# Performance work log

Measured on AMD Instinct MI355X. Metric: run time of the kernel, lower is better.

The kernel has to match this reference:

```python
import jax, jax.numpy as jnp
import numpy as np

N, E, EP = 200000, 1600000, 1000000
D, H1, CH, XDIM, L = 64, 256, 128, 20, 3


def gelu(x):
    return jax.nn.gelu(x, approximate=False)  # torch default = exact erf GELU


def dyt(x, w, b, a):
    # DynamicTanh (channels_last): w * tanh(alpha * x) + b
    return w * jnp.tanh(a * x) + b


def graph_norm(x, w, b, ms, eps=1e-5):
    # PyG GraphNorm with a single graph (batch = all zeros)
    mean = jnp.mean(x, axis=0, keepdims=True)
    xc = x - ms * mean
    var = jnp.mean(xc * xc, axis=0, keepdims=True)
    return w * xc / jnp.sqrt(var + eps) + b


def setup_inputs() -> dict:
    key = jax.random.key(0)
    ks = iter(jax.random.split(key, 64))
    nrm = lambda shape, s: jax.random.normal(next(ks), shape, jnp.float32) * s
    d = {}
    d['x_res'] = nrm((N, D), 1.0)
    s = 1.0 / np.sqrt(D)
    d['Wl'] = nrm((L, D, D), s); d['bl'] = jnp.zeros((L, D)); d['Wr'] = nrm((L, D, D), s)
    d['gn_w'] = jnp.ones((L, D)); d['gn_b'] = jnp.zeros((L, D)); d['gn_ms'] = jnp.ones((L, D))
    d['dyt1_w'] = jnp.ones((L * D,)); d['dyt1_b'] = jnp.zeros((L * D,)); d['dyt1_a'] = jnp.full((1,), 0.5, jnp.float32)
    d['lin1_w'] = nrm((L * D, H1), 1.0 / np.sqrt(L * D)); d['lin1_b'] = jnp.zeros((H1,))
    d['lin2_w'] = nrm((H1, H1), 1.0 / np.sqrt(H1)); d['lin2_b'] = jnp.zeros((H1,))
    d['lin3_w'] = nrm((H1, D), 1.0 / np.sqrt(H1)); d['lin3_b'] = jnp.zeros((D,))
    d['dyt2_w'] = jnp.ones((D,)); d['dyt2_b'] = jnp.zeros((D,)); d['dyt2_a'] = jnp.full((1,), 0.5, jnp.float32)
    d['adyt1_w'] = jnp.ones((2 * D,)); d['adyt1_b'] = jnp.zeros((2 * D,)); d['adyt1_a'] = jnp.full((1,), 0.5, jnp.float32)
    d['aa1_w'] = nrm((2 * D, H1), 1.0 / np.sqrt(2 * D)); d['aa1_b'] = jnp.zeros((H1,))
    d['aa2_w'] = nrm((H1, H1), 1.0 / np.sqrt(H1)); d['aa2_b'] = jnp.zeros((H1,))
    d['aa3_w'] = nrm((H1, H1), 1.0 / np.sqrt(H1)); d['aa3_b'] = jnp.zeros((H1,))
    d['adyt2_w'] = jnp.ones((H1,)); d['adyt2_b'] = jnp.zeros((H1,)); d['adyt2_a'] = jnp.full((1,), 0.5, jnp.float32)
    d['aa4_w'] = nrm((H1, XDIM), 1.0 / np.sqrt(H1)); d['aa4_b'] = jnp.zeros((XDIM,))
    d['c1_w'] = nrm((2 * D, CH), 1.0 / np.sqrt(2 * D)); d['c1_b'] = jnp.zeros((CH,))
    d['c2_w'] = nrm((CH, CH), 1.0 / np.sqrt(CH)); d['c2_b'] = jnp.zeros((CH,))
    d['c3_w'] = nrm((CH, 1), 1.0 / np.sqrt(CH)); d['c3_b'] = jnp.zeros((1,))
    d['edge_index'] = jax.random.randint(next(ks), (2, E), 0, N, dtype=jnp.int64 if jax.config.jax_enable_x64 else jnp.int32).astype(jnp.int32)
    d['contact_pred_index'] = jax.random.randint(next(ks), (2, EP), 0, N).astype(jnp.int32)
    return d


def reference(x_res, Wl, bl, Wr, gn_w, gn_b, gn_ms, dyt1_w, dyt1_b, dyt1_a,
              lin1_w, lin1_b, lin2_w, lin2_b, lin3_w, lin3_b, dyt2_w, dyt2_b, dyt2_a,
              adyt1_w, adyt1_b, adyt1_a, aa1_w, aa1_b, aa2_w, aa2_b, aa3_w, aa3_b,
              adyt2_w, adyt2_b, adyt2_a, aa4_w, aa4_b,
              c1_w, c1_b, c2_w, c2_b, c3_w, c3_b, edge_index, contact_pred_index):
    n = x_res.shape[0]
    src, dst = edge_index[0], edge_index[1]
    inz = x_res  # dropout is identity in eval / p~0
    x = x_res
    # in-degree for SAGE mean aggregation (clamped to 1 like PyG)
    deg = jnp.maximum(jax.ops.segment_sum(jnp.ones_like(src, dtype=x.dtype), dst, num_segments=n), 1.0)[:, None]
    xs = []
    for i in range(Wl.shape[0]):
        prev = x
        agg = jax.ops.segment_sum(x[src], dst, num_segments=n) / deg  # [N, D] mean of neighbor messages
        h = agg @ Wl[i] + bl[i] + x @ Wr[i]                            # SAGEConv: lin_l(aggr) + lin_r(x_dst)
        h = gelu(h)
        h = graph_norm(h, gn_w[i], gn_b[i], gn_ms[i])
        if i > 0:
            h = h + prev  # residual from layer 1 onward
        x = h
        xs.append(x)
    z = jnp.concatenate(xs, axis=1)  # JumpingKnowledge 'cat' -> [N, 3*D]
    z = dyt(z, dyt1_w, dyt1_b, dyt1_a)
    z = gelu(z @ lin1_w + lin1_b)
    z = gelu(z @ lin2_w + lin2_b)
    z = gelu(z @ lin3_w + lin3_b)
    z = dyt(z, dyt2_w, dyt2_b, dyt2_a)
    z = z + inz                                   # residual=True
    z = z / (jnp.linalg.norm(z, axis=1, keepdims=True) + 1e-10)  # normalize=True
    dec_in = jnp.concatenate([inz, z], axis=1)    # [N, 2*D]
    a = dyt(dec_in, adyt1_w, adyt1_b, adyt1_a)
    a = gelu(a @ aa1_w + aa1_b)
    a = gelu(a @ aa2_w + aa2_b)
    a = gelu(a @ aa3_w + aa3_b)
    a = dyt(a, adyt2_w, adyt2_b, adyt2_a)
    aa = jax.nn.log_softmax(a @ aa4_w + aa4_b, axis=1)  # [N, 20]
    ci, cj = contact_pred_index[0], contact_pred_index[1]
    ce = jnp.concatenate([z[ci], z[cj]], axis=1)  # [EP, 2*D] gather
    ce = gelu(ce @ c1_w + c1_b)
    ce = gelu(ce @ c2_w + c2_b)
    edge_probs = jax.nn.sigmoid((ce @ c3_w + c3_b)[:, 0])  # [EP]
    return aa, edge_probs
```

## Files before the change

### kernel.cpp

```cpp
#include <hip/hip_runtime.h>
#include <cstdint>
#include <cstddef>

constexpr int Nn  = 200000;
constexpr int Ee  = 1600000;
constexpr int EPp = 1000000;

typedef __attribute__((ext_vector_type(8))) short bf8_t;
typedef __attribute__((ext_vector_type(4))) float f4_t;

__device__ inline unsigned short f2bf(float f) {
  union { float f; unsigned u; } v; v.f = f;
  unsigned r = v.u + 0x7FFFu + ((v.u >> 16) & 1u);
  return (unsigned short)(r >> 16);
}
__device__ inline float bf2f(unsigned short u) {
  union { unsigned u; float f; } v; v.u = ((unsigned)u) << 16;
  return v.f;
}
__device__ inline float gelu_f(float v) {
  float u = v * fmaf(0.0356774081f, v * v, 0.7978845608f);
  float r = __builtin_amdgcn_rcpf(__expf(u + u) + 1.0f);
  return fmaf(-v, r, v);
}
__device__ inline float dyt_f(float x, float s2, float w, float b) {
  float r = __builtin_amdgcn_rcpf(__expf(s2 * x) + 1.0f);
  return fmaf(w, fmaf(-2.0f, r, 1.0f), b);
}


__global__ __launch_bounds__(256) void k_degi(const int* __restrict__ dst,
                                              int* __restrict__ cnt, int E) {
  int i = blockIdx.x * 256 + threadIdx.x;
  if (i < E) atomicAdd(&cnt[dst[i]], 1);
}

__global__ __launch_bounds__(256) void k_scan1(const int* __restrict__ in,
                                               int* __restrict__ out,
                                               int* __restrict__ bsum,
                                               float* __restrict__ rdeg, int n) {
  __shared__ int sd[256];
  int t = threadIdx.x;
  int base = blockIdx.x * 1024 + t * 4;
  int v[4]; int ts = 0;
  #pragma unroll
  for (int j = 0; j < 4; ++j) { v[j] = (base + j < n) ? in[base + j] : 0; ts += v[j]; }
  sd[t] = ts; __syncthreads();
  for (int off = 1; off < 256; off <<= 1) {
    int x = (t >= off) ? sd[t - off] : 0;
    __syncthreads();
    sd[t] += x;
    __syncthreads();
  }
  int excl = sd[t] - ts;
  #pragma unroll
  for (int j = 0; j < 4; ++j) {
    if (base + j < n) {
      out[base + j] = excl;
      rdeg[base + j] = 1.0f / (float)(v[j] > 1 ? v[j] : 1);
    }
    excl += v[j];
  }
  if (t == 255) bsum[blockIdx.x] = sd[255];
}

__global__ void k_scan2(int* bsum, int nb) {
  __shared__ int sd[256];
  int t = threadIdx.x;
  int v = (t < nb) ? bsum[t] : 0;
  sd[t] = v; __syncthreads();
  for (int off = 1; off < 256; off <<= 1) {
    int x = (t >= off) ? sd[t - off] : 0;
    __syncthreads();
    sd[t] += x;
    __syncthreads();
  }
  if (t < nb) bsum[t] = sd[t] - v;
}

__global__ __launch_bounds__(256) void k_scan3(const int* __restrict__ part,
                                               const int* __restrict__ bsum,
                                               int* __restrict__ rowptr,
                                               int* __restrict__ cursor,
                                               int n, int total) {
  int i = blockIdx.x * 256 + threadIdx.x;
  if (i == 0) rowptr[n] = total;
  if (i < n) { int v = part[i] + bsum[i >> 10]; rowptr[i] = v; cursor[i] = v; }
}

__global__ __launch_bounds__(256) void k_fill(const int* __restrict__ src,
                                              const int* __restrict__ dst,
                                              int* __restrict__ cursor,
                                              int* __restrict__ colidx, int E) {
  int e = blockIdx.x * 256 + threadIdx.x;
  if (e >= E) return;
  int pos = atomicAdd(&cursor[dst[e]], 1);
  colidx[pos] = src[e];
}

__global__ __launch_bounds__(256) void k_gather(const unsigned short* __restrict__ x, int ldx,
                                                const int* __restrict__ rowptr,
                                                const int* __restrict__ colidx,
                                                const float* __restrict__ rdeg,
                                                unsigned short* __restrict__ agg, int n) {
  int wave = threadIdx.x >> 6, lane = threadIdx.x & 63;
  int node = blockIdx.x * 4 + wave;
  if (node >= n) return;
  int grp = lane >> 3, c = (lane & 7) * 8;
  int r0 = rowptr[node], r1 = rowptr[node + 1];
  float s[8] = {0.f, 0.f, 0.f, 0.f, 0.f, 0.f, 0.f, 0.f};
  for (int j = r0 + grp; j < r1; j += 8) {
    bf8_t v = *(const bf8_t*)(x + (size_t)colidx[j] * ldx + c);
    #pragma unroll
    for (int jj = 0; jj < 8; ++jj) s[jj] += bf2f((unsigned short)v[jj]);
  }
  #pragma unroll
  for (int jj = 0; jj < 8; ++jj) {
    s[jj] += __shfl_xor(s[jj], 8, 64);
    s[jj] += __shfl_xor(s[jj], 16, 64);
    s[jj] += __shfl_xor(s[jj], 32, 64);
  }
  if (grp == 0) {
    float r = rdeg[node];
    bf8_t o;
    #pragma unroll
    for (int jj = 0; jj < 8; ++jj) o[jj] = (short)f2bf(s[jj] * r);
    *(bf8_t*)(agg + (size_t)node * 64 + c) = o;
  }
}


__global__ __launch_bounds__(256) void k_cvt(const float* __restrict__ in,
                                             unsigned short* __restrict__ out, int n) {
  int i = blockIdx.x * 256 + threadIdx.x;
  if (i < n) out[i] = f2bf(in[i]);
}

__device__ inline void wt3_elem(const float* __restrict__ W,
                                unsigned short* __restrict__ Wt,
                                int Np, int Nr, int i) {
  int kin = i & 31;
  int j = i >> 5;
  int n = j % Np, kb = j / Np;
  int k = kb * 32 + kin;
  float v = (n < Nr) ? W[(size_t)k * Nr + n] : 0.f;
  Wt[i] = f2bf(v);
}
__device__ inline void wt2_elem(const float* __restrict__ W,
                                unsigned short* __restrict__ Wt,
                                int K, int N, int i) {
  int n = i / K, k = i - n * K;
  float v = (n < N) ? W[(size_t)k * N + n] : 0.f;
  Wt[i] = f2bf(v);
}

__global__ __launch_bounds__(256) void k_wtall(
    const float* __restrict__ Wl, const float* __restrict__ Wr,
    const float* __restrict__ lin1_w, const float* __restrict__ lin2_w,
    const float* __restrict__ lin3_w,
    const float* __restrict__ aa1_w, const float* __restrict__ aa2_w,
    const float* __restrict__ aa3_w, const float* __restrict__ aa4_w,
    const float* __restrict__ c1_w, const float* __restrict__ c2_w,
    unsigned short* __restrict__ wt_sage,
    unsigned short* __restrict__ wt_lin1, unsigned short* __restrict__ wt_lin2,
    unsigned short* __restrict__ wt_lin3,
    unsigned short* __restrict__ wt_aa1, unsigned short* __restrict__ wt_aa2,
    unsigned short* __restrict__ wt_aa3, unsigned short* __restrict__ wt_aa4,
    unsigned short* __restrict__ wt_c1, unsigned short* __restrict__ wt_c2) {
  int i = blockIdx.x * 256 + threadIdx.x;
  if (i < 24576) {
    int l = i >> 13, r = i & 8191, n = r >> 7, k = r & 127;
    float v = (k < 64) ? Wl[l * 4096 + k * 64 + n] : Wr[l * 4096 + (k - 64) * 64 + n];
    wt_sage[i] = f2bf(v);
    return;
  }
  i -= 24576;
  if (i < 49152) { wt3_elem(lin1_w, wt_lin1, 256, 256, i); return; }  i -= 49152;
  if (i < 65536) { wt3_elem(lin2_w, wt_lin2, 256, 256, i); return; }  i -= 65536;
  if (i < 16384) { wt3_elem(lin3_w, wt_lin3, 64, 64, i);   return; }  i -= 16384;
  if (i < 32768) { wt3_elem(aa1_w, wt_aa1, 256, 256, i);   return; }  i -= 32768;
  if (i < 65536) { wt3_elem(aa2_w, wt_aa2, 256, 256, i);   return; }  i -= 65536;
  if (i < 65536) { wt3_elem(aa3_w, wt_aa3, 256, 256, i);   return; }  i -= 65536;
  if (i < 8192)  { wt3_elem(aa4_w, wt_aa4, 32, 20, i);     return; }  i -= 8192;
  if (i < 16384) { wt2_elem(c1_w, wt_c1, 128, 128, i);     return; }  i -= 16384;
  if (i < 16384) { wt2_elem(c2_w, wt_c2, 128, 128, i);     return; }
}

__global__ void k_statfin(float* stats, const float* __restrict__ ms_, int n) {
  int d = threadIdx.x;
  if (d < 64) {
    float invn = 1.0f / (float)n;
    float m  = stats[d] * invn;
    float e2 = stats[64 + d] * invn;
    float ms = ms_[d];
    float var = e2 - (2.0f * ms - ms * ms) * m * m;
    stats[128 + d] = ms * m;
    stats[192 + d] = rsqrtf(var + 1e-5f);
  }
}

__global__ __launch_bounds__(256) void k_norm(const float* __restrict__ h,
                                              const float* __restrict__ stats,
                                              const float* __restrict__ w,
                                              const float* __restrict__ b,
                                              unsigned short* __restrict__ zcol,
                                              const unsigned short* __restrict__ prev, int n) {
  int i = blockIdx.x * 256 + threadIdx.x;
  if (i >= n * 64) return;
  int r = i >> 6, d = i & 63;
  float v = (h[i] - stats[128 + d]) * stats[192 + d] * w[d] + b[d];
  if (prev) v += bf2f(prev[(size_t)r * 192 + d]);
  zcol[(size_t)r * 192 + d] = f2bf(v);
}

template <int NT>
__global__ __launch_bounds__(256) void mgemm(
    const void* __restrict__ A1, int lda1,
    const void* __restrict__ A2, int lda2, int K1, int a_bf16,
    const unsigned short* __restrict__ Wt,
    const float* __restrict__ bias,
    void* __restrict__ Cout, int ldc, int c_bf16, int act,
    float* __restrict__ stats_out,
    int M, int K, int N) {
  int lane = threadIdx.x & 63, wave = threadIdx.x >> 6;
  int quad = lane >> 4, col = lane & 15;
  int row0 = blockIdx.x * 128 + wave * 32;
  int n_base = blockIdx.y * NT * 16;

  __shared__ float ls[128];
  if (stats_out) {
    if (threadIdx.x < 128) ls[threadIdx.x] = 0.f;
    __syncthreads();
  }

  f4_t acc[2][NT];
  #pragma unroll
  for (int mt = 0; mt < 2; ++mt)
    #pragma unroll
    for (int nt = 0; nt < NT; ++nt) acc[mt][nt] = (f4_t)0.f;

  int gm[2];
  gm[0] = row0 + col;      if (gm[0] >= M) gm[0] = M - 1;
  gm[1] = row0 + 16 + col; if (gm[1] >= M) gm[1] = M - 1;

  for (int kc0 = 0; kc0 < K; kc0 += 32) {
    int kc = kc0 + quad * 8;
    bf8_t a[2];
    #pragma unroll
    for (int mt = 0; mt < 2; ++mt) {
      const void* src; size_t off;
      if (kc < K1) { src = A1; off = (size_t)gm[mt] * lda1 + kc; }
      else         { src = A2; off = (size_t)gm[mt] * lda2 + kc - K1; }
      if (a_bf16) {
        a[mt] = *(const bf8_t*)((const unsigned short*)src + off);
      } else {
        const float* p = (const float*)src + off;
        float4 f0 = *(const float4*)p;
        float4 f1 = *(const float4*)(p + 4);
        float ff[8] = {f0.x, f0.y, f0.z, f0.w, f1.x, f1.y, f1.z, f1.w};
        #pragma unroll
        for (int j = 0; j < 8; ++j) a[mt][j] = (short)f2bf(ff[j]);
      }
    }
    #pragma unroll
    for (int nt = 0; nt < NT; ++nt) {
      bf8_t b = *(const bf8_t*)(Wt + (size_t)(n_base + nt * 16 + col) * K + kc);
      acc[0][nt] = __builtin_amdgcn_mfma_f32_16x16x32_bf16(a[0], b, acc[0][nt], 0, 0, 0);
      acc[1][nt] = __builtin_amdgcn_mfma_f32_16x16x32_bf16(a[1], b, acc[1][nt], 0, 0, 0);
    }
  }

  #pragma unroll
  for (int nt = 0; nt < NT; ++nt) {
    int n = n_base + nt * 16 + col;
    float bs = (bias && n < N) ? bias[n] : 0.f;
    float sa = 0.f, s2a = 0.f;
    #pragma unroll
    for (int mt = 0; mt < 2; ++mt)
      #pragma unroll
      for (int r = 0; r < 4; ++r) {
        int row = row0 + mt * 16 + quad * 4 + r;
        if (row >= M || n >= N) continue;
        float v = acc[mt][nt][r] + bs;
        if (act) v = gelu_f(v);
        sa += v; s2a += v * v;
        if (c_bf16) ((unsigned short*)Cout)[(size_t)row * ldc + n] = f2bf(v);
        else        ((float*)Cout)[(size_t)row * ldc + n] = v;
      }
    if (stats_out && n < N) {
      atomicAdd(&ls[n & 63], sa);
      atomicAdd(&ls[64 + (n & 63)], s2a);
    }
  }
  if (stats_out) {
    __syncthreads();
    if (threadIdx.x < 128) atomicAdd(&stats_out[threadIdx.x], ls[threadIdx.x]);
  }
}

template <int K, bool DYT>
__device__ inline void node_gemm(unsigned short (*H)[264],
                                 const unsigned short* __restrict__ W,
                                 const float* __restrict__ bias,
                                 int wave, int quad, int col,
                                 const float* __restrict__ a2w,
                                 const float* __restrict__ a2b,
                                 const float* __restrict__ aal) {
  constexpr int KS = K >> 5;
  f4_t acc[4][4];
  #pragma unroll
  for (int mt = 0; mt < 4; ++mt)
    #pragma unroll
    for (int nt = 0; nt < 4; ++nt) acc[mt][nt] = (f4_t)0.f;

  const unsigned short* wp = W + (size_t)(wave * 64 + col) * 32 + quad * 8;
  bf8_t bc[4];
  #pragma unroll
  for (int nt = 0; nt < 4; ++nt)
    bc[nt] = *(const bf8_t*)(wp + (size_t)(nt * 16) * 32);

  #pragma unroll 2
  for (int s = 0; s < KS; ++s) {
    bf8_t am[4];
    #pragma unroll
    for (int mt = 0; mt < 4; ++mt)
      am[mt] = *(const bf8_t*)&H[mt * 16 + col][s * 32 + quad * 8];
    bf8_t bn[4];
    if (s + 1 < KS) {
      #pragma unroll
      for (int nt = 0; nt < 4; ++nt)
        bn[nt] = *(const bf8_t*)(wp + (size_t)((s + 1) * 256 + nt * 16) * 32);
    }
    #pragma unroll
    for (int nt = 0; nt < 4; ++nt)
      #pragma unroll
      for (int mt = 0; mt < 4; ++mt)
        acc[mt][nt] = __builtin_amdgcn_mfma_f32_16x16x32_bf16(am[mt], bc[nt], acc[mt][nt], 0, 0, 0);
    if (s + 1 < KS) {
      #pragma unroll
      for (int nt = 0; nt < 4; ++nt) bc[nt] = bn[nt];
    }
  }
  __syncthreads();
  float sa = DYT ? (2.0f * aal[0]) : 0.f;
  #pragma unroll
  for (int nt = 0; nt < 4; ++nt) {
    int n = wave * 64 + nt * 16 + col;
    float bs = bias[n];
    float w_ = DYT ? a2w[n] : 0.f;
    float b_ = DYT ? a2b[n] : 0.f;
    #pragma unroll
    for (int mt = 0; mt < 4; ++mt)
      #pragma unroll
      for (int r4 = 0; r4 < 4; ++r4) {
        float v = gelu_f(acc[mt][nt][r4] + bs);
        if (DYT) v = dyt_f(v, sa, w_, b_);
        H[mt * 16 + quad * 4 + r4][n] = f2bf(v);
      }
  }
  __syncthreads();
}

__global__ __launch_bounds__(256, 3) void k_node(
    const unsigned short* __restrict__ z_bf,
    const float* __restrict__ x_res,
    const float* __restrict__ d1w, const float* __restrict__ d1b, const float* __restrict__ d1a,
    const unsigned short* __restrict__ wt1, const float* __restrict__ b1,
    const unsigned short* __restrict__ wt2, const float* __restrict__ b2,
    const unsigned short* __restrict__ wt3, const float* __restrict__ b3,
    const float* __restrict__ d2w, const float* __restrict__ d2b, const float* __restrict__ d2a,
    const float* __restrict__ a1w, const float* __restrict__ a1b, const float* __restrict__ a1a,
    const unsigned short* __restrict__ wa1, const float* __restrict__ ba1,
    const unsigned short* __restrict__ wa2, const float* __restrict__ ba2,
    const unsigned short* __restrict__ wa3, const float* __restrict__ ba3,
    const float* __restrict__ a2w, const float* __restrict__ a2b, const float* __restrict__ a2a,
    const unsigned short* __restrict__ wa4, const float* __restrict__ ba4,
    unsigned short* __restrict__ zn_bf,
    float* __restrict__ out, int M) {
  __shared__ unsigned short H[64][264];
  __shared__ float fscr[64 * 4 + 64];
  int t = threadIdx.x;
  int lane = t & 63, wave = t >> 6;
  int quad = lane >> 4, col = lane & 15;
  int brow = blockIdx.x * 64;

  {
    int row = t >> 2, part = t & 3;
    int gr = brow + row; if (gr >= M) gr = M - 1;
    const unsigned short* zp = z_bf + (size_t)gr * 192 + part * 48;
    float s1 = 2.0f * d1a[0];
    #pragma unroll
    for (int j = 0; j < 6; ++j) {
      bf8_t v = *(const bf8_t*)(zp + j * 8);
      int k0 = part * 48 + j * 8;
      #pragma unroll
      for (int jj = 0; jj < 8; ++jj) {
        float f = bf2f((unsigned short)v[jj]);
        v[jj] = (short)f2bf(dyt_f(f, s1, d1w[k0 + jj], d1b[k0 + jj]));
      }
      *(bf8_t*)&H[row][k0] = v;
    }
  }
  __syncthreads();

  node_gemm<192, false>(H, wt1, b1, wave, quad, col, nullptr, nullptr, nullptr);
  node_gemm<256, false>(H, wt2, b2, wave, quad, col, nullptr, nullptr, nullptr);

  {
    f4_t a3[4];
    #pragma unroll
    for (int mt = 0; mt < 4; ++mt) a3[mt] = (f4_t)0.f;
    const unsigned short* wp3 = wt3 + (size_t)(wave * 16 + col) * 32 + quad * 8;
    bf8_t bc = *(const bf8_t*)(wp3);
    #pragma unroll 2
    for (int s = 0; s < 8; ++s) {
      bf8_t am[4];
      #pragma unroll
      for (int mt = 0; mt < 4; ++mt)
        am[mt] = *(const bf8_t*)&H[mt * 16 + col][s * 32 + quad * 8];
      bf8_t bn;
      if (s + 1 < 8) bn = *(const bf8_t*)(wp3 + (size_t)((s + 1) * 64) * 32);
      #pragma unroll
      for (int mt = 0; mt < 4; ++mt)
        a3[mt] = __builtin_amdgcn_mfma_f32_16x16x32_bf16(am[mt], bc, a3[mt], 0, 0, 0);
      if (s + 1 < 8) bc = bn;
    }
    __syncthreads();
    float* fb = (float*)H;
    float s2d = 2.0f * d2a[0];
    int n = wave * 16 + col;
    float bsn = b3[n], wd = d2w[n], bd = d2b[n];
    #pragma unroll
    for (int mt = 0; mt < 4; ++mt)
      #pragma unroll
      for (int r4 = 0; r4 < 4; ++r4) {
        int row = mt * 16 + quad * 4 + r4;
        int gr = brow + row; if (gr >= M) gr = M - 1;
        float g = gelu_f(a3[mt][r4] + bsn);
        float x = x_res[(size_t)gr * 64 + n];
        fb[row * 66 + n] = dyt_f(g, s2d, wd, bd) + x;
      }
    __syncthreads();
    int row = t >> 2, q = t & 3;
    float vreg[16];
    float s2 = 0.f;
    #pragma unroll
    for (int c16 = 0; c16 < 16; ++c16) {
      vreg[c16] = fb[row * 66 + q * 16 + c16];
      s2 += vreg[c16] * vreg[c16];
    }
    fscr[row * 4 + q] = s2;
    __syncthreads();
    if (t < 64)
      fscr[256 + t] = 1.0f / (sqrtf(fscr[t * 4] + fscr[t * 4 + 1] + fscr[t * 4 + 2] + fscr[t * 4 + 3]) + 1e-10f);
    __syncthreads();
    float sa1 = 2.0f * a1a[0];
    float inv = fscr[256 + row];
    int gr = brow + row;
    int grc = (gr >= M) ? (M - 1) : gr;
    #pragma unroll
    for (int c16 = 0; c16 < 16; ++c16) {
      int c = q * 16 + c16;
      float zv = vreg[c16] * inv;
      if (gr < M) zn_bf[(size_t)gr * 64 + c] = f2bf(zv);
      float x = x_res[(size_t)grc * 64 + c];
      H[row][64 + c] = f2bf(dyt_f(zv, sa1, a1w[64 + c], a1b[64 + c]));
      H[row][c]      = f2bf(dyt_f(x,  sa1, a1w[c],      a1b[c]));
    }
    __syncthreads();
  }

  node_gemm<128, false>(H, wa1, ba1, wave, quad, col, nullptr, nullptr, nullptr);
  node_gemm<256, false>(H, wa2, ba2, wave, quad, col, nullptr, nullptr, nullptr);
  node_gemm<256, true >(H, wa3, ba3, wave, quad, col, a2w, a2b, a2a);

  {
    f4_t a4[2];
    a4[0] = (f4_t)0.f; a4[1] = (f4_t)0.f;
    const unsigned short* wp4 = wa4 + (size_t)col * 32 + quad * 8;
    bf8_t bc[2];
    bc[0] = *(const bf8_t*)(wp4);
    bc[1] = *(const bf8_t*)(wp4 + (size_t)(16) * 32);
    #pragma unroll 2
    for (int s = 0; s < 8; ++s) {
      bf8_t am = *(const bf8_t*)&H[wave * 16 + col][s * 32 + quad * 8];
      bf8_t bn[2];
      if (s + 1 < 8) {
        bn[0] = *(const bf8_t*)(wp4 + (size_t)((s + 1) * 32) * 32);
        bn[1] = *(const bf8_t*)(wp4 + (size_t)((s + 1) * 32 + 16) * 32);
      }
      #pragma unroll
      for (int nt = 0; nt < 2; ++nt)
        a4[nt] = __builtin_amdgcn_mfma_f32_16x16x32_bf16(am, bc[nt], a4[nt], 0, 0, 0);
      if (s + 1 < 8) { bc[0] = bn[0]; bc[1] = bn[1]; }
    }
    float val[2][4];
    #pragma unroll
    for (int nt = 0; nt < 2; ++nt) {
      int n = nt * 16 + col;
      float bsv = (n < 20) ? ba4[n] : 0.f;
      #pragma unroll
      for (int r4 = 0; r4 < 4; ++r4) val[nt][r4] = a4[nt][r4] + bsv;
    }
    bool v1 = (col < 4);
    #pragma unroll
    for (int r4 = 0; r4 < 4; ++r4) {
      float m = val[0][r4];
      if (v1) m = fmaxf(m, val[1][r4]);
      m = fmaxf(m, __shfl_xor(m, 1, 64));
      m = fmaxf(m, __shfl_xor(m, 2, 64));
      m = fmaxf(m, __shfl_xor(m, 4, 64));
      m = fmaxf(m, __shfl_xor(m, 8, 64));
      float se = __expf(val[0][r4] - m) + (v1 ? __expf(val[1][r4] - m) : 0.f);
      se += __shfl_xor(se, 1, 64);
      se += __shfl_xor(se, 2, 64);
      se += __shfl_xor(se, 4, 64);
      se += __shfl_xor(se, 8, 64);
      float ls = __logf(se) + m;
      int row = brow + wave * 16 + quad * 4 + r4;
      if (row < M) {
        out[(size_t)row * 20 + col] = val[0][r4] - ls;
        if (v1) out[(size_t)row * 20 + 16 + col] = val[1][r4] - ls;
      }
    }
  }
}

__global__ __launch_bounds__(256) void k_edge(
    const unsigned short* __restrict__ zn_bf,
    const int* __restrict__ ci, const int* __restrict__ cj,
    const unsigned short* __restrict__ w1t, const float* __restrict__ b1,
    const unsigned short* __restrict__ w2t, const float* __restrict__ b2,
    const float* __restrict__ w3, const float* __restrict__ b3,
    float* __restrict__ out, int M) {
  __shared__ unsigned short h1s[4][16][136];
  int lane = threadIdx.x & 63, wave = threadIdx.x >> 6;
  int quad = lane >> 4, col = lane & 15;
  unsigned short (*h1)[136] = h1s[wave];
  int ntiles = (M + 63) >> 6;
  float b3v = b3[0];

  int tile = blockIdx.x;
  bf8_t afrag[4];
  if (tile < ntiles) {
    int r = tile * 64 + wave * 16 + col; if (r >= M) r = M - 1;
    const unsigned short* p0 = zn_bf + (size_t)ci[r] * 64;
    const unsigned short* p1 = zn_bf + (size_t)cj[r] * 64;
    afrag[0] = *(const bf8_t*)(p0 + quad * 8);
    afrag[1] = *(const bf8_t*)(p0 + 32 + quad * 8);
    afrag[2] = *(const bf8_t*)(p1 + quad * 8);
    afrag[3] = *(const bf8_t*)(p1 + 32 + quad * 8);
  }

  for (; tile < ntiles; tile += gridDim.x) {
    f4_t acc[8];
    #pragma unroll
    for (int nt = 0; nt < 8; ++nt) acc[nt] = (f4_t)0.f;
    #pragma unroll
    for (int s = 0; s < 4; ++s) {
      int kf = s * 32 + quad * 8;
      #pragma unroll
      for (int nt = 0; nt < 8; ++nt) {
        bf8_t b = *(const bf8_t*)(w1t + (size_t)(nt * 16 + col) * 128 + kf);
        acc[nt] = __builtin_amdgcn_mfma_f32_16x16x32_bf16(afrag[s], b, acc[nt], 0, 0, 0);
      }
    }

    int nxt = tile + gridDim.x;
    bf8_t nfrag[4];
    bool has_next = (nxt < ntiles);
    if (has_next) {
      int r = nxt * 64 + wave * 16 + col; if (r >= M) r = M - 1;
      const unsigned short* p0 = zn_bf + (size_t)ci[r] * 64;
      const unsigned short* p1 = zn_bf + (size_t)cj[r] * 64;
      nfrag[0] = *(const bf8_t*)(p0 + quad * 8);
      nfrag[1] = *(const bf8_t*)(p0 + 32 + quad * 8);
      nfrag[2] = *(const bf8_t*)(p1 + quad * 8);
      nfrag[3] = *(const bf8_t*)(p1 + 32 + quad * 8);
    }

    #pragma unroll
    for (int nt = 0; nt < 8; ++nt) {
      float bs = b1[nt * 16 + col];
      #pragma unroll
      for (int r4 = 0; r4 < 4; ++r4)
        h1[quad * 4 + r4][nt * 16 + col] = f2bf(gelu_f(acc[nt][r4] + bs));
    }

    f4_t a2[8];
    #pragma unroll
    for (int nt = 0; nt < 8; ++nt) a2[nt] = (f4_t)0.f;
    #pragma unroll
    for (int s = 0; s < 4; ++s) {
      int kc = s * 32 + quad * 8;
      bf8_t a0 = *(const bf8_t*)&h1[col][kc];
      #pragma unroll
      for (int nt = 0; nt < 8; ++nt) {
        bf8_t b = *(const bf8_t*)(w2t + (size_t)(nt * 16 + col) * 128 + kc);
        a2[nt] = __builtin_amdgcn_mfma_f32_16x16x32_bf16(a0, b, a2[nt], 0, 0, 0);
      }
    }
    float p[4] = {0.f, 0.f, 0.f, 0.f};
    #pragma unroll
    for (int nt = 0; nt < 8; ++nt) {
      float bs = b2[nt * 16 + col];
      float wv = w3[nt * 16 + col];
      #pragma unroll
      for (int r4 = 0; r4 < 4; ++r4)
        p[r4] += gelu_f(a2[nt][r4] + bs) * wv;
    }
    #pragma unroll
    for (int r4 = 0; r4 < 4; ++r4) {
      float s = p[r4];
      s += __shfl_xor(s, 1, 64);
      s += __shfl_xor(s, 2, 64);
      s += __shfl_xor(s, 4, 64);
      s += __shfl_xor(s, 8, 64);
      if (col == 0) {
        int row = tile * 64 + wave * 16 + quad * 4 + r4;
        if (row < M) out[row] = __builtin_amdgcn_rcpf(1.0f + __expf(-(s + b3v)));
      }
    }

    if (has_next) {
      afrag[0] = nfrag[0]; afrag[1] = nfrag[1];
      afrag[2] = nfrag[2]; afrag[3] = nfrag[3];
    }
  }
}

extern "C" void kernel_launch(void* const* d_in, const int* in_sizes, int n_in,
                              void* d_out, int out_size, void* d_ws, size_t ws_size,
                              hipStream_t stream) {
  const float* x_res  = (const float*)d_in[0];
  const float* Wl     = (const float*)d_in[1];
  const float* bl     = (const float*)d_in[2];
  const float* Wr     = (const float*)d_in[3];
  const float* gn_w   = (const float*)d_in[4];
  const float* gn_b   = (const float*)d_in[5];
  const float* gn_ms  = (const float*)d_in[6];
  const float* dyt1_w = (const float*)d_in[7];
  const float* dyt1_b = (const float*)d_in[8];
  const float* dyt1_a = (const float*)d_in[9];
  const float* lin1_w = (const float*)d_in[10];
  const float* lin1_b = (const float*)d_in[11];
  const float* lin2_w = (const float*)d_in[12];
  const float* lin2_b = (const float*)d_in[13];
  const float* lin3_w = (const float*)d_in[14];
  const float* lin3_b = (const float*)d_in[15];
  const float* dyt2_w = (const float*)d_in[16];
  const float* dyt2_b = (const float*)d_in[17];
  const float* dyt2_a = (const float*)d_in[18];
  const float* adyt1_w = (const float*)d_in[19];
  const float* adyt1_b = (const float*)d_in[20];
  const float* adyt1_a = (const float*)d_in[21];
  const float* aa1_w  = (const float*)d_in[22];
  const float* aa1_b  = (const float*)d_in[23];
  const float* aa2_w  = (const float*)d_in[24];
  const float* aa2_b  = (const float*)d_in[25];
  const float* aa3_w  = (const float*)d_in[26];
  const float* aa3_b  = (const float*)d_in[27];
  const float* adyt2_w = (const float*)d_in[28];
  const float* adyt2_b = (const float*)d_in[29];
  const float* adyt2_a = (const float*)d_in[30];
  const float* aa4_w  = (const float*)d_in[31];
  const float* aa4_b  = (const float*)d_in[32];
  const float* c1_w   = (const float*)d_in[33];
  const float* c1_b   = (const float*)d_in[34];
  const float* c2_w   = (const float*)d_in[35];
  const float* c2_b   = (const float*)d_in[36];
  const float* c3_w   = (const float*)d_in[37];
  const float* c3_b   = (const float*)d_in[38];
  const int*   edge   = (const int*)d_in[39];
  const int*   contact = (const int*)d_in[40];

  const size_t N = (size_t)Nn;
  const size_t ws_floats = ws_size / 4;

  float* ws    = (float*)d_ws;
  float* rdeg  = ws;
  float* hbuf  = rdeg + N;
  unsigned short* z_bf  = (unsigned short*)(hbuf + 64 * N);
  unsigned short* zn_bf = z_bf + 192 * N;
  float* stats = (float*)(zn_bf + 64 * N);
  unsigned short* wt_sage = (unsigned short*)(stats + 768);
  unsigned short* wt_lin1 = wt_sage + 3 * 64 * 128;
  unsigned short* wt_lin2 = wt_lin1 + 256 * 192;
  unsigned short* wt_lin3 = wt_lin2 + 256 * 256;
  unsigned short* wt_aa1  = wt_lin3 + 64 * 256;
  unsigned short* wt_aa2  = wt_aa1 + 256 * 128;
  unsigned short* wt_aa3  = wt_aa2 + 256 * 256;
  unsigned short* wt_aa4  = wt_aa3 + 256 * 256;
  unsigned short* wt_c1   = wt_aa4 + 32 * 256;
  unsigned short* wt_c2   = wt_c1 + 128 * 128;
  unsigned short* wt_end  = wt_c2 + 128 * 128;
  float* pool  = (float*)((((uintptr_t)wt_end + 15) & ~(uintptr_t)15));
  const size_t persist = (size_t)(pool - ws);

  const size_t gnn_need = 32 * N + N + (N + 1) + N + (size_t)Ee + 256;
  if (ws_floats < persist + gnn_need) return;

  unsigned short* agg_bf = (unsigned short*)pool;
  int* cnt     = (int*)(pool + 32 * N);
  int* rowptr  = cnt + N;
  int* cursor  = rowptr + N + 1;
  int* colidx  = cursor + N;
  int* bsum    = colidx + Ee;

  const int* esrc = edge;
  const int* edst = edge + Ee;

  hipMemsetAsync(cnt, 0, N * sizeof(int), stream);
  hipMemsetAsync(stats, 0, 768 * sizeof(float), stream);
  k_degi<<<(Ee + 255) / 256, 256, 0, stream>>>(edst, cnt, Ee);
  const int nb = (Nn + 1023) / 1024;
  k_scan1<<<nb, 256, 0, stream>>>(cnt, cursor, bsum, rdeg, Nn);
  k_scan2<<<1, 256, 0, stream>>>(bsum, nb);
  k_scan3<<<(Nn + 255) / 256, 256, 0, stream>>>(cursor, bsum, rowptr, cursor, Nn, Ee);
  k_fill<<<(Ee + 255) / 256, 256, 0, stream>>>(esrc, edst, cursor, colidx, Ee);

  k_wtall<<<(360448 + 255) / 256, 256, 0, stream>>>(
      Wl, Wr, lin1_w, lin2_w, lin3_w, aa1_w, aa2_w, aa3_w, aa4_w, c1_w, c2_w,
      wt_sage, wt_lin1, wt_lin2, wt_lin3, wt_aa1, wt_aa2, wt_aa3, wt_aa4,
      wt_c1, wt_c2);

  k_cvt<<<(int)((N * 64 + 255) / 256), 256, 0, stream>>>(x_res, zn_bf, (int)(N * 64));

  for (int l = 0; l < 3; ++l) {
    const unsigned short* xi = (l == 0) ? zn_bf : (z_bf + (size_t)(l - 1) * 64);
    int ldx = (l == 0) ? 64 : 192;
    float* stats_l = stats + (size_t)l * 256;
    k_gather<<<(Nn + 3) / 4, 256, 0, stream>>>(xi, ldx, rowptr, colidx, rdeg, agg_bf, Nn);
    mgemm<4><<<dim3((Nn + 127) / 128, 1), 256, 0, stream>>>(
        agg_bf, 64, xi, ldx, 64, 1,
        wt_sage + (size_t)l * 8192, bl + l * 64, hbuf, 64, 0, 1, stats_l, Nn, 128, 64);
    k_statfin<<<1, 64, 0, stream>>>(stats_l, gn_ms + l * 64, Nn);
    k_norm<<<(Nn * 64) / 256, 256, 0, stream>>>(hbuf, stats_l, gn_w + l * 64, gn_b + l * 64,
                                                z_bf + (size_t)l * 64,
                                                (l > 0) ? (z_bf + (size_t)(l - 1) * 64) : nullptr, Nn);
  }

  k_node<<<(Nn + 63) / 64, 256, 0, stream>>>(
      z_bf, x_res,
      dyt1_w, dyt1_b, dyt1_a, wt_lin1, lin1_b, wt_lin2, lin2_b, wt_lin3, lin3_b,
      dyt2_w, dyt2_b, dyt2_a,
      adyt1_w, adyt1_b, adyt1_a, wt_aa1, aa1_b, wt_aa2, aa2_b, wt_aa3, aa3_b,
      adyt2_w, adyt2_b, adyt2_a, wt_aa4, aa4_b,
      zn_bf, (float*)d_out, Nn);

  float* eout = (float*)d_out + (size_t)Nn * 20;
  k_edge<<<2048, 256, 0, stream>>>(zn_bf, contact, contact + EPp,
      wt_c1, c1_b, wt_c2, c2_b, c3_w, c3_b, eout, EPp);
}
```

Before: 1.451 ms.

## Split k_node across eight waves with half-width column tiles per wave

Raises k_node from 256 to 512 threads per block. Each wave now computes 32 output columns instead of 64 in the MLP GEMMs, and the lin3, normalization and dyt prologue stages are re-partitioned across eight waves. The aim is more waves in flight per CU and fewer accumulator registers per thread, to hide LDS and weight-load latency. In exchange, each weight column tile is loaded by more waves, the block has more barrier participants, and the final aa4 stage leaves half the waves idle.

Measured after the change: 1.436 ms. Within noise of the previous version (-1.0%).

```diff
diff --git a/kernel.cpp b/kernel.cpp
--- a/kernel.cpp
+++ b/kernel.cpp
@@ -299,24 +299,24 @@
 }
 
 template <int K, bool DYT>
-__device__ inline void node_gemm(unsigned short (*H)[264],
-                                 const unsigned short* __restrict__ W,
-                                 const float* __restrict__ bias,
-                                 int wave, int quad, int col,
-                                 const float* __restrict__ a2w,
-                                 const float* __restrict__ a2b,
-                                 const float* __restrict__ aal) {
+__device__ inline void node_gemm8(unsigned short (*H)[264],
+                                  const unsigned short* __restrict__ W,
+                                  const float* __restrict__ bias,
+                                  int wave, int quad, int col,
+                                  const float* __restrict__ a2w,
+                                  const float* __restrict__ a2b,
+                                  const float* __restrict__ aal) {
   constexpr int KS = K >> 5;
-  f4_t acc[4][4];
+  f4_t acc[4][2];
   #pragma unroll
   for (int mt = 0; mt < 4; ++mt)
     #pragma unroll
-    for (int nt = 0; nt < 4; ++nt) acc[mt][nt] = (f4_t)0.f;
-
-  const unsigned short* wp = W + (size_t)(wave * 64 + col) * 32 + quad * 8;
-  bf8_t bc[4];
+    for (int nt = 0; nt < 2; ++nt) acc[mt][nt] = (f4_t)0.f;
+
+  const unsigned short* wp = W + (size_t)(wave * 32 + col) * 32 + quad * 8;
+  bf8_t bc[2];
   #pragma unroll
-  for (int nt = 0; nt < 4; ++nt)
+  for (int nt = 0; nt < 2; ++nt)
     bc[nt] = *(const bf8_t*)(wp + (size_t)(nt * 16) * 32);
 
   #pragma unroll 2
@@ -325,27 +325,27 @@
     #pragma unroll
     for (int mt = 0; mt < 4; ++mt)
       am[mt] = *(const bf8_t*)&H[mt * 16 + col][s * 32 + quad * 8];
-    bf8_t bn[4];
+    bf8_t bn[2];
     if (s + 1 < KS) {
       #pragma unroll
-      for (int nt = 0; nt < 4; ++nt)
+      for (int nt = 0; nt < 2; ++nt)
         bn[nt] = *(const bf8_t*)(wp + (size_t)((s + 1) * 256 + nt * 16) * 32);
     }
     #pragma unroll
-    for (int nt = 0; nt < 4; ++nt)
+    for (int nt = 0; nt < 2; ++nt)
       #pragma unroll
       for (int mt = 0; mt < 4; ++mt)
         acc[mt][nt] = __builtin_amdgcn_mfma_f32_16x16x32_bf16(am[mt], bc[nt], acc[mt][nt], 0, 0, 0);
     if (s + 1 < KS) {
       #pragma unroll
-      for (int nt = 0; nt < 4; ++nt) bc[nt] = bn[nt];
+      for (int nt = 0; nt < 2; ++nt) bc[nt] = bn[nt];
     }
   }
   __syncthreads();
   float sa = DYT ? (2.0f * aal[0]) : 0.f;
   #pragma unroll
-  for (int nt = 0; nt < 4; ++nt) {
-    int n = wave * 64 + nt * 16 + col;
+  for (int nt = 0; nt < 2; ++nt) {
+    int n = wave * 32 + nt * 16 + col;
     float bs = bias[n];
     float w_ = DYT ? a2w[n] : 0.f;
     float b_ = DYT ? a2b[n] : 0.f;
@@ -361,7 +361,7 @@
   __syncthreads();
 }
 
-__global__ __launch_bounds__(256, 3) void k_node(
+__global__ __launch_bounds__(512, 4) void k_node(
     const unsigned short* __restrict__ z_bf,
     const float* __restrict__ x_res,
     const float* __restrict__ d1w, const float* __restrict__ d1b, const float* __restrict__ d1a,
@@ -378,21 +378,21 @@
     unsigned short* __restrict__ zn_bf,
     float* __restrict__ out, int M) {
   __shared__ unsigned short H[64][264];
-  __shared__ float fscr[64 * 4 + 64];
+  __shared__ float fscr[512 + 64];
   int t = threadIdx.x;
   int lane = t & 63, wave = t >> 6;
   int quad = lane >> 4, col = lane & 15;
   int brow = blockIdx.x * 64;
 
   {
-    int row = t >> 2, part = t & 3;
+    int row = t >> 3, part = t & 7;
     int gr = brow + row; if (gr >= M) gr = M - 1;
-    const unsigned short* zp = z_bf + (size_t)gr * 192 + part * 48;
+    const unsigned short* zp = z_bf + (size_t)gr * 192 + part * 24;
     float s1 = 2.0f * d1a[0];
     #pragma unroll
-    for (int j = 0; j < 6; ++j) {
+    for (int j = 0; j < 3; ++j) {
       bf8_t v = *(const bf8_t*)(zp + j * 8);
-      int k0 = part * 48 + j * 8;
+      int k0 = part * 24 + j * 8;
       #pragma unroll
       for (int jj = 0; jj < 8; ++jj) {
         float f = bf2f((unsigned short)v[jj]);
@@ -403,65 +403,69 @@
   }
   __syncthreads();
 
-  node_gemm<192, false>(H, wt1, b1, wave, quad, col, nullptr, nullptr, nullptr);
-  node_gemm<256, false>(H, wt2, b2, wave, quad, col, nullptr, nullptr, nullptr);
+  node_gemm8<192, false>(H, wt1, b1, wave, quad, col, nullptr, nullptr, nullptr);
+  node_gemm8<256, false>(H, wt2, b2, wave, quad, col, nullptr, nullptr, nullptr);
 
   {
-    f4_t a3[4];
-    #pragma unroll
-    for (int mt = 0; mt < 4; ++mt) a3[mt] = (f4_t)0.f;
-    const unsigned short* wp3 = wt3 + (size_t)(wave * 16 + col) * 32 + quad * 8;
+    int mhalf = wave >> 2, ctile = wave & 3;
+    f4_t a3[2];
+    a3[0] = (f4_t)0.f; a3[1] = (f4_t)0.f;
+    const unsigned short* wp3 = wt3 + (size_t)(ctile * 16 + col) * 32 + quad * 8;
     bf8_t bc = *(const bf8_t*)(wp3);
     #pragma unroll 2
     for (int s = 0; s < 8; ++s) {
-      bf8_t am[4];
-      #pragma unroll
-      for (int mt = 0; mt < 4; ++mt)
-        am[mt] = *(const bf8_t*)&H[mt * 16 + col][s * 32 + quad * 8];
+      bf8_t am[2];
+      #pragma unroll
+      for (int i = 0; i < 2; ++i)
+        am[i] = *(const bf8_t*)&H[(mhalf * 2 + i) * 16 + col][s * 32 + quad * 8];
       bf8_t bn;
       if (s + 1 < 8) bn = *(const bf8_t*)(wp3 + (size_t)((s + 1) * 64) * 32);
       #pragma unroll
-      for (int mt = 0; mt < 4; ++mt)
-        a3[mt] = __builtin_amdgcn_mfma_f32_16x16x32_bf16(am[mt], bc, a3[mt], 0, 0, 0);
+      for (int i = 0; i < 2; ++i)
+        a3[i] = __builtin_amdgcn_mfma_f32_16x16x32_bf16(am[i], bc, a3[i], 0, 0, 0);
       if (s + 1 < 8) bc = bn;
     }
     __syncthreads();
     float* fb = (float*)H;
     float s2d = 2.0f * d2a[0];
-    int n = wave * 16 + col;
+    int n = ctile * 16 + col;
     float bsn = b3[n], wd = d2w[n], bd = d2b[n];
     #pragma unroll
-    for (int mt = 0; mt < 4; ++mt)
+    for (int i = 0; i < 2; ++i)
       #pragma unroll
       for (int r4 = 0; r4 < 4; ++r4) {
-        int row = mt * 16 + quad * 4 + r4;
+        int row = (mhalf * 2 + i) * 16 + quad * 4 + r4;
         int gr = brow + row; if (gr >= M) gr = M - 1;
-        float g = gelu_f(a3[mt][r4] + bsn);
+        float g = gelu_f(a3[i][r4] + bsn);
         float x = x_res[(size_t)gr * 64 + n];
         fb[row * 66 + n] = dyt_f(g, s2d, wd, bd) + x;
       }
     __syncthreads();
-    int row = t >> 2, q = t & 3;
-    float vreg[16];
+    int row = t >> 3, q = t & 7;
+    float vreg[8];
     float s2 = 0.f;
     #pragma unroll
-    for (int c16 = 0; c16 < 16; ++c16) {
-      vreg[c16] = fb[row * 66 + q * 16 + c16];
-      s2 += vreg[c16] * vreg[c16];
-    }
-    fscr[row * 4 + q] = s2;
-    __syncthreads();
-    if (t < 64)
-      fscr[256 + t] = 1.0f / (sqrtf(fscr[t * 4] + fscr[t * 4 + 1] + fscr[t * 4 + 2] + fscr[t * 4 + 3]) + 1e-10f);
+    for (int c8 = 0; c8 < 8; ++c8) {
+      vreg[c8] = fb[row * 66 + q * 8 + c8];
+      s2 += vreg[c8] * vreg[c8];
+    }
+    fscr[row * 8 + q] = s2;
+    __syncthreads();
+    if (t < 64) {
+      float ssum = 0.f;
+      #pragma unroll
+      for (int j = 0; j < 8; ++j) ssum += fscr[t * 8 + j];
+      fscr[512 + t] = 1.0f / (sqrtf(ssum) + 1e-10f);
+    }
     __syncthreads();
     float sa1 = 2.0f * a1a[0];
-    float inv = fscr[256 + row];
+    float inv = fscr[512 + row];
     int gr = brow + row;
     int grc = (gr >= M) ? (M - 1) : gr;
     #pragma unroll
-    for (int c16 = 0; c16 < 16; ++c16) {
-      int c = q * 16 + c16;
-      float zv = vreg[c16] * inv;
+    for (int c8 = 0; c8 < 8; ++c8) {
+      int c = q * 8 + c8;
+      float zv = vreg[c8] * inv;
       if (gr < M) zn_bf[(size_t)gr * 64 + c] = f2bf(zv);
       float x = x_res[(size_t)grc * 64 + c];
       H[row][64 + c] = f2bf(dyt_f(zv, sa1, a1w[64 + c], a1b[64 + c]));
@@ -470,11 +474,11 @@
     __syncthreads();
   }
 
-  node_gemm<128, false>(H, wa1, ba1, wave, quad, col, nullptr, nullptr, nullptr);
-  node_gemm<256, false>(H, wa2, ba2, wave, quad, col, nullptr, nullptr, nullptr);
-  node_gemm<256, true >(H, wa3, ba3, wave, quad, col, a2w, a2b, a2a);
-
-  {
+  node_gemm8<128, false>(H, wa1, ba1, wave, quad, col, nullptr, nullptr, nullptr);
+  node_gemm8<256, false>(H, wa2, ba2, wave, quad, col, nullptr, nullptr, nullptr);
+  node_gemm8<256, true >(H, wa3, ba3, wave, quad, col, a2w, a2b, a2a);
+
+  if (wave < 4) {
     f4_t a4[2];
     a4[0] = (f4_t)0.f; a4[1] = (f4_t)0.f;
     const unsigned short* wp4 = wa4 + (size_t)col * 32 + quad * 8;
@@ -740,7 +744,7 @@
                                                 (l > 0) ? (z_bf + (size_t)(l - 1) * 64) : nullptr, Nn);
   }
 
-  k_node<<<(Nn + 63) / 64, 256, 0, stream>>>(
+  k_node<<<(Nn + 63) / 64, 512, 0, stream>>>(
       z_bf, x_res,
       dyt1_w, dyt1_b, dyt1_a, wt_lin1, lin1_b, wt_lin2, lin2_b, wt_lin3, lin3_b,
       dyt2_w, dyt2_b, dyt2_a,
```
